# Optimization experiments

Measured on AMD Instinct MI355X. Metric: run time of the kernel, lower is better.

## Reference

```python
import jax, jax.numpy as jnp
import numpy as np

B, S, D, H, DFF = 8, 1024, 1024, 16, 4096
DK = D // H
NEG = -1000000000.0


def layernorm(x, g, b, eps=1e-5):
    mu = jnp.mean(x, axis=-1, keepdims=True)
    var = jnp.mean((x - mu) ** 2, axis=-1, keepdims=True)
    return (x - mu) / jnp.sqrt(var + eps) * g + b


def setup_inputs() -> dict:
    key = jax.random.key(0)
    ks = jax.random.split(key, 16)
    s = 0.02
    inp = {
        "x": jax.random.normal(ks[0], (B, S, D), jnp.float32),
        "binary_mask": jax.random.randint(ks[1], (B, S), 0, 2, jnp.int32),
        # per-head projections stacked: [H, D, DK]
        "Wq": jax.random.normal(ks[2], (H, D, DK), jnp.float32) * s,
        "bq": jnp.zeros((H, DK), jnp.float32),
        "Wk": jax.random.normal(ks[3], (H, D, DK), jnp.float32) * s,
        "bk": jnp.zeros((H, DK), jnp.float32),
        "Wv": jax.random.normal(ks[4], (H, D, DK), jnp.float32) * s,
        "bv": jnp.zeros((H, DK), jnp.float32),
        "Wo": jax.random.normal(ks[5], (D, D), jnp.float32) * s,
        "bo": jnp.zeros((D,), jnp.float32),
        "ga": jnp.ones((D,), jnp.float32),
        "ba": jnp.zeros((D,), jnp.float32),
        "W1": jax.random.normal(ks[6], (D, DFF), jnp.float32) * s,
        "b1": jnp.zeros((DFF,), jnp.float32),
        "W2": jax.random.normal(ks[7], (DFF, D), jnp.float32) * s,
        "b2": jnp.zeros((D,), jnp.float32),
        "gf": jnp.ones((D,), jnp.float32),
        "bf": jnp.zeros((D,), jnp.float32),
    }
    return inp


def encoder_fwd(x, binary_mask, Wq, bq, Wk, bk, Wv, bv, Wo, bo, ga, ba, W1, b1, W2, b2, gf, bf):
    # --- multi-head self-attention (heads vectorized over h axis) ---
    q = jnp.einsum("bsd,hdk->bhsk", x, Wq) + bq[None, :, None, :]
    k = jnp.einsum("bsd,hdk->bhsk", x, Wk) + bk[None, :, None, :]
    v = jnp.einsum("bsd,hdk->bhsk", x, Wv) + bv[None, :, None, :]
    score = jnp.einsum("bhik,bhjk->bhij", q, k) / jnp.sqrt(jnp.float32(DK))
    # mask: binary_mask is over KEY positions, broadcast over query dim
    score = score + jnp.where(binary_mask[:, None, None, :] == 0, NEG, 0.0)
    # NOTE: original code softmaxes over dim=1 of [B,Sq,Sk] -> the QUERY axis
    probs = jax.nn.softmax(score, axis=2)
    ctx = jnp.einsum("bhij,bhjk->bhik", probs, v)  # [B,H,S,DK]
    ctx = jnp.transpose(ctx, (0, 2, 1, 3)).reshape(x.shape[0], x.shape[1], D)
    attn_out = ctx @ Wo + bo
    y = layernorm(x + attn_out, ga, ba)
    # --- FFN ---
    h = jax.nn.relu(y @ W1 + b1)
    ffn_out = h @ W2 + b2
    return layernorm(y + ffn_out, gf, bf)


def reference(x, binary_mask, Wq, bq, Wk, bk, Wv, bv, Wo, bo, ga, ba, W1, b1, W2, b2, gf, bf):
    return encoder_fwd(x, binary_mask, Wq, bq, Wk, bk, Wv, bv, Wo, bo, ga, ba, W1, b1, W2, b2, gf, bf)
```

## Files before the change

### kernel.cpp

```cpp
#include <hip/hip_runtime.h>
#include <hip/hip_bf16.h>

typedef __bf16 bf16;
typedef __bf16 bf16x8 __attribute__((ext_vector_type(8)));
typedef __bf16 bf16x4 __attribute__((ext_vector_type(4)));
typedef float  f32x4  __attribute__((ext_vector_type(4)));

#define NB 8
#define NS 1024
#define ND 1024
#define NH 16
#define NDK 64
#define NDFF 4096

static __device__ __forceinline__ f32x4 mfma16(bf16x8 a, bf16x8 b, f32x4 c) {
    return __builtin_amdgcn_mfma_f32_16x16x32_bf16(a, b, c, 0, 0, 0);
}

#define GLDS(g, l) __builtin_amdgcn_global_load_lds( \
    (const __attribute__((address_space(1))) void*)(g), \
    (__attribute__((address_space(3))) void*)(l), 16, 0, 0)

__global__ __launch_bounds__(256) void cvt_x(const float* __restrict__ in,
                                             bf16* __restrict__ out, int n4)
{
    int idx = blockIdx.x * 256 + threadIdx.x;
    if (idx >= n4) return;
    float4 v = ((const float4*)in)[idx];
    bf16x4 o = { (bf16)v.x, (bf16)v.y, (bf16)v.z, (bf16)v.w };
    ((bf16x4*)out)[idx] = o;
}

__global__ __launch_bounds__(256) void prep_transpose(
    const float* __restrict__ Wq, const float* __restrict__ Wk, const float* __restrict__ Wv,
    const float* __restrict__ Wo, const float* __restrict__ W1, const float* __restrict__ W2,
    bf16* __restrict__ wqkvT, bf16* __restrict__ WoT,
    bf16* __restrict__ W1T, bf16* __restrict__ W2T)
{
    __shared__ float T[64][65];
    int bid = blockIdx.x;
    const float* src; bf16* dst; int srcLd, dstLd, tR, tC; bool scale = false;
    if (bid < 768) {
        int mat = bid >> 4, ty = bid & 15;
        int h = mat & 15, type = mat >> 4;
        const float* W = (type == 0) ? Wq : (type == 1 ? Wk : Wv);
        src = W + (size_t)h * ND * NDK;
        srcLd = NDK; tR = ty * 64; tC = 0;
        dst = wqkvT + ((size_t)type * 1024 + h * 64) * ND;
        dstLd = ND;
        scale = (type == 0);
    } else if (bid < 1024) {
        int b2 = bid - 768; int ty = b2 >> 4, tx = b2 & 15;
        src = Wo; srcLd = ND; tR = ty * 64; tC = tx * 64; dst = WoT; dstLd = ND;
    } else if (bid < 2048) {
        int b2 = bid - 1024; int ty = b2 >> 6, tx = b2 & 63;
        src = W1; srcLd = NDFF; tR = ty * 64; tC = tx * 64; dst = W1T; dstLd = ND;
    } else {
        int b2 = bid - 2048; int ty = b2 >> 4, tx = b2 & 15;
        src = W2; srcLd = ND; tR = ty * 64; tC = tx * 64; dst = W2T; dstLd = NDFF;
    }
    int t = threadIdx.x;
    int c0 = t & 63, r0 = t >> 6;
    #pragma unroll
    for (int rr = 0; rr < 16; rr++) {
        int row = rr * 4 + r0;
        T[row][c0] = src[(size_t)(tR + row) * srcLd + tC + c0];
    }
    __syncthreads();
    #pragma unroll
    for (int cc = 0; cc < 16; cc++) {
        int col = cc * 4 + r0;
        float v = T[c0][col];
        if (scale) v *= 0.125f;
        dst[(size_t)(tC + col) * dstLd + tR + c0] = (bf16)v;
    }
}

__global__ void prep_bias(const float* __restrict__ bq, const float* __restrict__ bk,
                          const float* __restrict__ bv, float* __restrict__ bqkv)
{
    int n = blockIdx.x * 256 + threadIdx.x;
    if (n >= 3072) return;
    int type = n >> 10, hk = n & 1023;
    const float* bb = (type == 0) ? bq : (type == 1 ? bk : bv);
    float v = bb[hk];
    if (type == 0) v *= 0.125f;
    bqkv[n] = v;
}

__device__ __forceinline__ void gemm_bt_core(
    const bf16* __restrict__ A, const bf16* __restrict__ BT, int K,
    int rowBase, int colBase, f32x4 (&acc)[4][4], bf16* As, bf16* Bs)
{
    const int tid = threadIdx.x;
    const int lane = tid & 63, wid = tid >> 6;
    const int wr = (wid >> 1) * 64, wc = (wid & 1) * 64;
    const int lrow = lane & 15, lq = lane >> 4;
    const int srow = wid * 32 + (lane >> 3);
    const int gblk = (lane & 7) ^ ((lane >> 3) & 7);
    const bf16* Arow = A + (size_t)(rowBase + srow) * K + gblk * 8;
    const bf16* Brow = BT + (size_t)(colBase + srow) * K + gblk * 8;
    const int co0 = ((lq) ^ (lrow & 7)) * 8;
    const int co1 = ((4 + lq) ^ (lrow & 7)) * 8;
    f32x4 zz = {0.f, 0.f, 0.f, 0.f};
    #pragma unroll
    for (int i = 0; i < 4; i++)
        #pragma unroll
        for (int j = 0; j < 4; j++) acc[i][j] = zz;
    for (int k0 = 0; k0 < K; k0 += 64) {
        __syncthreads();
        #pragma unroll
        for (int it = 0; it < 4; it++)
            GLDS(Arow + (size_t)it * 8 * K + k0, As + (wid * 32 + it * 8) * 64);
        #pragma unroll
        for (int it = 0; it < 4; it++)
            GLDS(Brow + (size_t)it * 8 * K + k0, Bs + (wid * 32 + it * 8) * 64);
        __syncthreads();
        #pragma unroll
        for (int kh = 0; kh < 2; kh++) {
            const int co = kh ? co1 : co0;
            bf16x8 af[4], bfr[4];
            #pragma unroll
            for (int tt = 0; tt < 4; tt++) {
                af[tt]  = *(const bf16x8*)&As[(wr + tt * 16 + lrow) * 64 + co];
                bfr[tt] = *(const bf16x8*)&Bs[(wc + tt * 16 + lrow) * 64 + co];
            }
            #pragma unroll
            for (int i = 0; i < 4; i++)
                #pragma unroll
                for (int j = 0; j < 4; j++)
                    acc[i][j] = mfma16(af[i], bfr[j], acc[i][j]);
        }
    }
}

__global__ __launch_bounds__(256) void g1_qkv(
    const bf16* __restrict__ x, const bf16* __restrict__ wqkvT, const float* __restrict__ bqkv,
    bf16* __restrict__ Q, bf16* __restrict__ Kb, bf16* __restrict__ Vb)
{
    __shared__ bf16 As[128 * 64], Bs[128 * 64];
    f32x4 acc[4][4];
    int rowBase = blockIdx.x * 128, colBase = blockIdx.y * 128;
    gemm_bt_core(x, wqkvT, ND, rowBase, colBase, acc, As, Bs);
    const int tid = threadIdx.x, lane = tid & 63, wid = tid >> 6;
    const int wr = (wid >> 1) * 64, wc = (wid & 1) * 64, lrow = lane & 15, lq = lane >> 4;
    #pragma unroll
    for (int j = 0; j < 4; j++) {
        int gcol = colBase + wc + j * 16 + lrow;
        float bias = bqkv[gcol];
        int type = gcol >> 10, h = (gcol >> 6) & 15, kk = gcol & 63;
        bf16* dst = (type == 0) ? Q : (type == 1 ? Kb : Vb);
        #pragma unroll
        for (int i = 0; i < 4; i++) {
            #pragma unroll
            for (int r = 0; r < 4; r++) {
                int grow = rowBase + wr + i * 16 + lq * 4 + r;
                int b = grow >> 10, s = grow & 1023;
                dst[((size_t)(b * NH + h) * NS + s) * NDK + kk] = (bf16)(acc[i][j][r] + bias);
            }
        }
    }
}

__global__ __launch_bounds__(256) void vt_trans(
    const bf16* __restrict__ Vb, bf16* __restrict__ Vt)
{
    __shared__ bf16 T[64 * 72];
    int bh = blockIdx.y, s0 = blockIdx.x * 64;
    const bf16* src = Vb + ((size_t)bh * NS + s0) * NDK;
    int tid = threadIdx.x;
    #pragma unroll
    for (int it = 0; it < 2; it++) {
        int g = tid + it * 256;
        int row = g >> 3, c = (g & 7) * 8;
        *(bf16x8*)&T[row * 72 + c] = *(const bf16x8*)&src[row * NDK + c];
    }
    __syncthreads();
    #pragma unroll
    for (int it = 0; it < 2; it++) {
        int g = tid + it * 256;
        int kk = g >> 3, sc = (g & 7) * 8;
        bf16x8 v;
        #pragma unroll
        for (int t = 0; t < 8; t++) v[t] = T[(sc + t) * 72 + kk];
        *(bf16x8*)&Vt[((size_t)bh * NDK + kk) * NS + s0 + sc] = v;
    }
}

__global__ __launch_bounds__(256) void g2_stats(
    const bf16* __restrict__ Q, const bf16* __restrict__ Kb,
    const int* __restrict__ mask, float2* __restrict__ alpha)
{
    __shared__ bf16 Qs[128 * 64];
    int bh = blockIdx.y, b = bh >> 4;
    int jBase = blockIdx.x * 128;
    const bf16* Kp = Kb + (size_t)bh * NS * NDK;
    const bf16* Qp = Q + (size_t)bh * NS * NDK;
    const int tid = threadIdx.x, lane = tid & 63, wid = tid >> 6;
    const int lrow = lane & 15, lq = lane >> 4;
    bf16x8 kf[2][2];
    #pragma unroll
    for (int jt = 0; jt < 2; jt++)
        #pragma unroll
        for (int kh = 0; kh < 2; kh++)
            kf[jt][kh] = *(const bf16x8*)&Kp[(size_t)(jBase + wid * 32 + jt * 16 + lrow) * NDK + kh * 32 + lq * 8];
    const int srow = lane >> 3;
    const int gblk = (lane & 7) ^ srow;
    float Lacc[2][4];
    #pragma unroll
    for (int jt = 0; jt < 2; jt++)
        #pragma unroll
        for (int r = 0; r < 4; r++) Lacc[jt][r] = 0.f;
    f32x4 zz = {0.f, 0.f, 0.f, 0.f};
    for (int i0 = 0; i0 < NS; i0 += 128) {
        __syncthreads();
        #pragma unroll
        for (int it = 0; it < 4; it++)
            GLDS(Qp + (size_t)(i0 + wid * 32 + it * 8 + srow) * NDK + gblk * 8,
                 Qs + (wid * 32 + it * 8) * 64);
        __syncthreads();
        #pragma unroll
        for (int it = 0; it < 8; it++) {
            bf16x8 qb[2];
            #pragma unroll
            for (int kh = 0; kh < 2; kh++)
                qb[kh] = *(const bf16x8*)&Qs[(it * 16 + lrow) * 64 + ((kh * 4 + lq) ^ (lrow & 7)) * 8];
            #pragma unroll
            for (int jt = 0; jt < 2; jt++) {
                f32x4 s = mfma16(kf[jt][0], qb[0], zz);
                s = mfma16(kf[jt][1], qb[1], s);
                #pragma unroll
                for (int r = 0; r < 4; r++) Lacc[jt][r] += __expf(s[r]);
            }
        }
    }
    #pragma unroll
    for (int jt = 0; jt < 2; jt++) {
        #pragma unroll
        for (int r = 0; r < 4; r++) {
            float v = Lacc[jt][r];
            v += __shfl_xor(v, 1); v += __shfl_xor(v, 2);
            v += __shfl_xor(v, 4); v += __shfl_xor(v, 8);
            if (lrow == 0) {
                int j = jBase + wid * 32 + jt * 16 + lq * 4 + r;
                int m = mask[b * NS + j];
                float2 ac;
                ac.x = m ? 1.f / v : 0.f;
                ac.y = m ? 0.f : (1.f / 1024.f);
                alpha[(size_t)bh * NS + j] = ac;
            }
        }
    }
}

__global__ __launch_bounds__(256) void g3_ctx(
    const bf16* __restrict__ Q, const bf16* __restrict__ Kb, const bf16* __restrict__ Vt,
    const float2* __restrict__ alpha, bf16* __restrict__ ctx)
{
    __shared__ bf16 Ks[64 * 64];
    __shared__ bf16 Vs[64 * 64];
    __shared__ bf16 Ps[4 * 64 * 64];
    int bh = blockIdx.y, iBase = blockIdx.x * 256;
    int b = bh >> 4, h = bh & 15;
    const bf16* Qp = Q + (size_t)bh * NS * NDK;
    const bf16* Kp = Kb + (size_t)bh * NS * NDK;
    const bf16* Vp = Vt + (size_t)bh * NDK * NS;
    const float2* al = alpha + (size_t)bh * NS;
    const int tid = threadIdx.x, lane = tid & 63, wid = tid >> 6;
    const int lrow = lane & 15, lq = lane >> 4;
    const int iw = iBase + wid * 64;
    bf16x8 qf[4][2];
    #pragma unroll
    for (int it = 0; it < 4; it++)
        #pragma unroll
        for (int kh = 0; kh < 2; kh++)
            qf[it][kh] = *(const bf16x8*)&Qp[(size_t)(iw + it * 16 + lrow) * NDK + kh * 32 + lq * 8];
    const int srow = lane >> 3;
    const int gblk = (lane & 7) ^ srow;
    f32x4 cacc[4][4];
    f32x4 zz = {0.f, 0.f, 0.f, 0.f};
    #pragma unroll
    for (int it = 0; it < 4; it++)
        #pragma unroll
        for (int kt = 0; kt < 4; kt++) cacc[it][kt] = zz;
    bf16* Pw = Ps + wid * 64 * 64;
    for (int j0 = 0; j0 < NS; j0 += 64) {
        __syncthreads();
        #pragma unroll
        for (int it = 0; it < 2; it++)
            GLDS(Kp + (size_t)(j0 + wid * 16 + it * 8 + srow) * NDK + gblk * 8,
                 Ks + (wid * 16 + it * 8) * 64);
        #pragma unroll
        for (int it = 0; it < 2; it++)
            GLDS(Vp + (size_t)(wid * 16 + it * 8 + srow) * NS + j0 + gblk * 8,
                 Vs + (wid * 16 + it * 8) * 64);
        __syncthreads();
        bf16x8 kb[4][2];
        #pragma unroll
        for (int jt = 0; jt < 4; jt++)
            #pragma unroll
            for (int kh = 0; kh < 2; kh++)
                kb[jt][kh] = *(const bf16x8*)&Ks[(jt * 16 + lrow) * 64 + ((kh * 4 + lq) ^ (lrow & 7)) * 8];
        #pragma unroll
        for (int jt = 0; jt < 4; jt++) {
            float2 acj[4];
            #pragma unroll
            for (int r = 0; r < 4; r++) acj[r] = al[j0 + jt * 16 + lq * 4 + r];
            #pragma unroll
            for (int it = 0; it < 4; it++) {
                f32x4 s = mfma16(kb[jt][0], qf[it][0], zz);
                s = mfma16(kb[jt][1], qf[it][1], s);
                bf16x4 pv;
                #pragma unroll
                for (int r = 0; r < 4; r++)
                    pv[r] = (bf16)(acj[r].x * __expf(s[r]) + acj[r].y);
                int i = it * 16 + lrow;
                int jb = jt * 2 + (lq >> 1);
                *(bf16x4*)&Pw[i * 64 + ((jb ^ (i & 7)) * 8) + (lq & 1) * 4] = pv;
            }
        }
        bf16x8 vb[4][2];
        #pragma unroll
        for (int kt = 0; kt < 4; kt++)
            #pragma unroll
            for (int kh = 0; kh < 2; kh++)
                vb[kt][kh] = *(const bf16x8*)&Vs[(kt * 16 + lrow) * 64 + ((kh * 4 + lq) ^ (lrow & 7)) * 8];
        #pragma unroll
        for (int it = 0; it < 4; it++) {
            bf16x8 pa[2];
            #pragma unroll
            for (int kh = 0; kh < 2; kh++)
                pa[kh] = *(const bf16x8*)&Pw[(it * 16 + lrow) * 64 + ((kh * 4 + lq) ^ (lrow & 7)) * 8];
            #pragma unroll
            for (int kt = 0; kt < 4; kt++) {
                cacc[it][kt] = mfma16(pa[0], vb[kt][0], cacc[it][kt]);
                cacc[it][kt] = mfma16(pa[1], vb[kt][1], cacc[it][kt]);
            }
        }
    }
    #pragma unroll
    for (int kt = 0; kt < 4; kt++) {
        int col = h * NDK + kt * 16 + lrow;
        #pragma unroll
        for (int it = 0; it < 4; it++) {
            #pragma unroll
            for (int r = 0; r < 4; r++) {
                int i = iw + it * 16 + lq * 4 + r;
                ctx[(size_t)(b * NS + i) * ND + col] = (bf16)cacc[it][kt][r];
            }
        }
    }
}

__global__ __launch_bounds__(256) void g4_proj(
    const bf16* __restrict__ ctx, const bf16* __restrict__ WoT, const float* __restrict__ bo,
    const bf16* __restrict__ xb, bf16* __restrict__ t1b)
{
    __shared__ bf16 As[128 * 64], Bs[128 * 64];
    f32x4 acc[4][4];
    int rowBase = blockIdx.x * 128, colBase = blockIdx.y * 128;
    gemm_bt_core(ctx, WoT, ND, rowBase, colBase, acc, As, Bs);
    const int tid = threadIdx.x, lane = tid & 63, wid = tid >> 6;
    const int wr = (wid >> 1) * 64, wc = (wid & 1) * 64, lrow = lane & 15, lq = lane >> 4;
    #pragma unroll
    for (int j = 0; j < 4; j++) {
        int gcol = colBase + wc + j * 16 + lrow;
        float bias = bo[gcol];
        #pragma unroll
        for (int i = 0; i < 4; i++) {
            #pragma unroll
            for (int r = 0; r < 4; r++) {
                int grow = rowBase + wr + i * 16 + lq * 4 + r;
                float v = acc[i][j][r] + bias + (float)xb[(size_t)grow * ND + gcol];
                t1b[(size_t)grow * ND + gcol] = (bf16)v;
            }
        }
    }
}

__global__ __launch_bounds__(256) void g5_ffn1(
    const bf16* __restrict__ y, const bf16* __restrict__ W1T, const float* __restrict__ b1,
    bf16* __restrict__ hb)
{
    __shared__ bf16 As[128 * 64], Bs[128 * 64];
    f32x4 acc[4][4];
    int rowBase = blockIdx.x * 128, colBase = blockIdx.y * 128;
    gemm_bt_core(y, W1T, ND, rowBase, colBase, acc, As, Bs);
    const int tid = threadIdx.x, lane = tid & 63, wid = tid >> 6;
    const int wr = (wid >> 1) * 64, wc = (wid & 1) * 64, lrow = lane & 15, lq = lane >> 4;
    #pragma unroll
    for (int j = 0; j < 4; j++) {
        int gcol = colBase + wc + j * 16 + lrow;
        float bias = b1[gcol];
        #pragma unroll
        for (int i = 0; i < 4; i++) {
            #pragma unroll
            for (int r = 0; r < 4; r++) {
                int grow = rowBase + wr + i * 16 + lq * 4 + r;
                float v = fmaxf(acc[i][j][r] + bias, 0.f);
                hb[(size_t)grow * NDFF + gcol] = (bf16)v;
            }
        }
    }
}

__global__ __launch_bounds__(256) void g6_ffn2(
    const bf16* __restrict__ hb, const bf16* __restrict__ W2T, const float* __restrict__ b2,
    const bf16* __restrict__ yb, bf16* __restrict__ zb)
{
    __shared__ bf16 As[128 * 64], Bs[128 * 64];
    f32x4 acc[4][4];
    int rowBase = blockIdx.x * 128, colBase = blockIdx.y * 128;
    gemm_bt_core(hb, W2T, NDFF, rowBase, colBase, acc, As, Bs);
    const int tid = threadIdx.x, lane = tid & 63, wid = tid >> 6;
    const int wr = (wid >> 1) * 64, wc = (wid & 1) * 64, lrow = lane & 15, lq = lane >> 4;
    #pragma unroll
    for (int j = 0; j < 4; j++) {
        int gcol = colBase + wc + j * 16 + lrow;
        float bias = b2[gcol];
        #pragma unroll
        for (int i = 0; i < 4; i++) {
            #pragma unroll
            for (int r = 0; r < 4; r++) {
                int grow = rowBase + wr + i * 16 + lq * 4 + r;
                float v = acc[i][j][r] + bias + (float)yb[(size_t)grow * ND + gcol];
                zb[(size_t)grow * ND + gcol] = (bf16)v;
            }
        }
    }
}

__global__ __launch_bounds__(256) void ln_kernel(
    const bf16* __restrict__ in, bf16* __restrict__ outb, float* __restrict__ outf,
    const float* __restrict__ g, const float* __restrict__ bb)
{
    int row = blockIdx.x, tid = threadIdx.x;
    const bf16* p = in + (size_t)row * ND;
    bf16x4 v4 = *(const bf16x4*)&p[tid * 4];
    float vv[4] = {(float)v4[0], (float)v4[1], (float)v4[2], (float)v4[3]};
    float s = vv[0] + vv[1] + vv[2] + vv[3];
    float q = vv[0]*vv[0] + vv[1]*vv[1] + vv[2]*vv[2] + vv[3]*vv[3];
    #pragma unroll
    for (int m = 1; m < 64; m <<= 1) { s += __shfl_xor(s, m); q += __shfl_xor(q, m); }
    __shared__ float rs[4], rq[4];
    int wid = tid >> 6, lane = tid & 63;
    if (lane == 0) { rs[wid] = s; rq[wid] = q; }
    __syncthreads();
    s = rs[0] + rs[1] + rs[2] + rs[3];
    q = rq[0] + rq[1] + rq[2] + rq[3];
    float mean = s * (1.f / 1024.f);
    float var = q * (1.f / 1024.f) - mean * mean;
    float rstd = 1.f / sqrtf(var + 1e-5f);
    float4 of;
    bf16x4 ob;
    #pragma unroll
    for (int k = 0; k < 4; k++) {
        int col = tid * 4 + k;
        float yv = (vv[k] - mean) * rstd * g[col] + bb[col];
        ((float*)&of)[k] = yv;
        ob[k] = (bf16)yv;
    }
    if (outb) *(bf16x4*)&outb[(size_t)row * ND + tid * 4] = ob;
    if (outf) ((float4*)(outf + (size_t)row * ND))[tid] = of;
}

extern "C" void kernel_launch(void* const* d_in, const int* in_sizes, int n_in,
                              void* d_out, int out_size, void* d_ws, size_t ws_size,
                              hipStream_t stream)
{
    const float* x    = (const float*)d_in[0];
    const int*   mask = (const int*)d_in[1];
    const float* Wq   = (const float*)d_in[2];
    const float* bq   = (const float*)d_in[3];
    const float* Wk   = (const float*)d_in[4];
    const float* bk   = (const float*)d_in[5];
    const float* Wv   = (const float*)d_in[6];
    const float* bv   = (const float*)d_in[7];
    const float* Wo   = (const float*)d_in[8];
    const float* bo   = (const float*)d_in[9];
    const float* ga   = (const float*)d_in[10];
    const float* ba   = (const float*)d_in[11];
    const float* W1   = (const float*)d_in[12];
    const float* b1   = (const float*)d_in[13];
    const float* W2   = (const float*)d_in[14];
    const float* b2   = (const float*)d_in[15];
    const float* gf   = (const float*)d_in[16];
    const float* bfb  = (const float*)d_in[17];

    size_t off = 0;
    auto alloc = [&](size_t n) { char* p = (char*)d_ws + off; off += (n + 255) & ~(size_t)255; return (void*)p; };
    bf16*   wqkvT = (bf16*)  alloc((size_t)3072 * 1024 * 2);
    bf16*   WoT   = (bf16*)  alloc((size_t)1024 * 1024 * 2);
    bf16*   W1T   = (bf16*)  alloc((size_t)4096 * 1024 * 2);
    bf16*   W2T   = (bf16*)  alloc((size_t)1024 * 4096 * 2);
    float*  bqkv  = (float*) alloc(3072 * 4);
    float2* alpha = (float2*)alloc((size_t)NB * NH * NS * 8);
    bf16*   xb    = (bf16*)  alloc((size_t)8192 * 1024 * 2);
    bf16*   ub    = (bf16*)  alloc((size_t)8192 * 4096 * 2);
    bf16*   Qb    = ub;
    bf16*   Kb    = ub + (size_t)8192 * 1024;
    bf16*   Vt    = ub + (size_t)2 * 8192 * 1024;
    bf16*   ctx   = ub + (size_t)3 * 8192 * 1024;
    bf16*   hb    = ub;
    bf16*   t1b   = (bf16*)  alloc((size_t)8192 * 1024 * 2);
    bf16*   Vb    = t1b;
    bf16*   zb    = t1b;
    bf16*   yb    = (bf16*)  alloc((size_t)8192 * 1024 * 2);

    cvt_x<<<8192, 256, 0, stream>>>(x, xb, 8192 * 1024 / 4);
    prep_transpose<<<3072, 256, 0, stream>>>(Wq, Wk, Wv, Wo, W1, W2, wqkvT, WoT, W1T, W2T);
    prep_bias<<<12, 256, 0, stream>>>(bq, bk, bv, bqkv);
    g1_qkv<<<dim3(64, 24), 256, 0, stream>>>(xb, wqkvT, bqkv, Qb, Kb, Vb);
    vt_trans<<<dim3(16, 128), 256, 0, stream>>>(Vb, Vt);
    g2_stats<<<dim3(8, 128), 256, 0, stream>>>(Qb, Kb, mask, alpha);
    g3_ctx<<<dim3(4, 128), 256, 0, stream>>>(Qb, Kb, Vt, alpha, ctx);
    g4_proj<<<dim3(64, 8), 256, 0, stream>>>(ctx, WoT, bo, xb, t1b);
    ln_kernel<<<8192, 256, 0, stream>>>(t1b, yb, nullptr, ga, ba);
    g5_ffn1<<<dim3(64, 32), 256, 0, stream>>>(yb, W1T, b1, hb);
    g6_ffn2<<<dim3(64, 8), 256, 0, stream>>>(hb, W2T, b2, yb, zb);
    ln_kernel<<<8192, 256, 0, stream>>>(zb, nullptr, (float*)d_out, gf, bfb);
}
```

Baseline: 508.8 us.

## Rewrite GEMM core with 256-row tiles, double-buffered LDS, and XCD-aware block swizzle

Replaces the 128x128 single-buffered GEMM core with a 256xBN (128 or 256) tile run by 512 threads. The next K-tile is prefetched into a second LDS buffer while MFMA clusters interleave with LDS fragment reads under explicit barriers and raised priority. Block indices are remapped with an 8-way swizzle meant to improve L2 locality across XCDs. The aim is to hide global load latency and raise data reuse per tile, at the cost of more LDS and registers, fewer blocks for the smaller GEMMs, and a more fragile barrier schedule.

```diff
diff --git a/kernel.cpp b/kernel.cpp
--- a/kernel.cpp
+++ b/kernel.cpp
@@ -88,73 +88,129 @@
     bqkv[n] = v;
 }
 
-__device__ __forceinline__ void gemm_bt_core(
+template<int BN>
+__device__ __forceinline__ void gemm256_core(
     const bf16* __restrict__ A, const bf16* __restrict__ BT, int K,
-    int rowBase, int colBase, f32x4 (&acc)[4][4], bf16* As, bf16* Bs)
-{
+    int rowBase, int colBase, f32x4 (&acc)[8][BN / 64],
+    bf16* As, bf16* Bs)
+{
+    constexpr int NJ = BN / 128;
+    constexpr int ABUF = 256 * 64;
+    constexpr int BBUF = BN * 64;
     const int tid = threadIdx.x;
     const int lane = tid & 63, wid = tid >> 6;
-    const int wr = (wid >> 1) * 64, wc = (wid & 1) * 64;
+    const int wm = wid >> 2, wn = wid & 3;
     const int lrow = lane & 15, lq = lane >> 4;
-    const int srow = wid * 32 + (lane >> 3);
-    const int gblk = (lane & 7) ^ ((lane >> 3) & 7);
-    const bf16* Arow = A + (size_t)(rowBase + srow) * K + gblk * 8;
-    const bf16* Brow = BT + (size_t)(colBase + srow) * K + gblk * 8;
-    const int co0 = ((lq) ^ (lrow & 7)) * 8;
+    const int srow = lane >> 3, gblk = (lane & 7) ^ srow;
+    const int co0 = (lq ^ (lrow & 7)) * 8;
     const int co1 = ((4 + lq) ^ (lrow & 7)) * 8;
+
     f32x4 zz = {0.f, 0.f, 0.f, 0.f};
     #pragma unroll
-    for (int i = 0; i < 4; i++)
-        #pragma unroll
-        for (int j = 0; j < 4; j++) acc[i][j] = zz;
-    for (int k0 = 0; k0 < K; k0 += 64) {
-        __syncthreads();
-        #pragma unroll
-        for (int it = 0; it < 4; it++)
-            GLDS(Arow + (size_t)it * 8 * K + k0, As + (wid * 32 + it * 8) * 64);
-        #pragma unroll
-        for (int it = 0; it < 4; it++)
-            GLDS(Brow + (size_t)it * 8 * K + k0, Bs + (wid * 32 + it * 8) * 64);
-        __syncthreads();
-        #pragma unroll
-        for (int kh = 0; kh < 2; kh++) {
-            const int co = kh ? co1 : co0;
-            bf16x8 af[4], bfr[4];
-            #pragma unroll
-            for (int tt = 0; tt < 4; tt++) {
-                af[tt]  = *(const bf16x8*)&As[(wr + tt * 16 + lrow) * 64 + co];
-                bfr[tt] = *(const bf16x8*)&Bs[(wc + tt * 16 + lrow) * 64 + co];
-            }
-            #pragma unroll
-            for (int i = 0; i < 4; i++)
-                #pragma unroll
-                for (int j = 0; j < 4; j++)
-                    acc[i][j] = mfma16(af[i], bfr[j], acc[i][j]);
-        }
-    }
-}
-
-__global__ __launch_bounds__(256) void g1_qkv(
+    for (int i = 0; i < 8; i++)
+        #pragma unroll
+        for (int j = 0; j < 2 * NJ; j++) acc[i][j] = zz;
+
+    const bf16* Ag = A  + (size_t)(rowBase + wid * 8 + srow) * K + gblk * 8;
+    const bf16* Bg = BT + (size_t)(colBase + wid * 8 + srow) * K + gblk * 8;
+
+#define STAGE256(kt, bi) do { \
+    const bf16* a_ = Ag + (size_t)(kt) * 64; \
+    _Pragma("unroll") \
+    for (int r_ = 0; r_ < 4; r_++) \
+        GLDS(a_ + (size_t)r_ * 64 * K, As + (bi) * ABUF + (r_ * 64 + wid * 8) * 64); \
+    const bf16* b_ = Bg + (size_t)(kt) * 64; \
+    _Pragma("unroll") \
+    for (int r_ = 0; r_ < BN / 64; r_++) \
+        GLDS(b_ + (size_t)r_ * 64 * K, Bs + (bi) * BBUF + (r_ * 64 + wid * 8) * 64); \
+} while (0)
+
+#define READ_A(MS) \
+    _Pragma("unroll") \
+    for (int i_ = 0; i_ < 4; i_++) { \
+        int ro_ = (wm * 128 + (MS) * 64 + i_ * 16 + lrow) * 64; \
+        af[i_][0] = *(const bf16x8*)&Ab[ro_ + co0]; \
+        af[i_][1] = *(const bf16x8*)&Ab[ro_ + co1]; \
+    }
+
+#define READ_B(NS_) \
+    _Pragma("unroll") \
+    for (int j_ = 0; j_ < NJ; j_++) { \
+        int ro_ = (wn * (BN / 4) + (NS_) * (BN / 8) + j_ * 16 + lrow) * 64; \
+        bfr[j_][0] = *(const bf16x8*)&Bb[ro_ + co0]; \
+        bfr[j_][1] = *(const bf16x8*)&Bb[ro_ + co1]; \
+    }
+
+#define MFMA_CLUSTER(IOFF, JOFF) do { \
+    __builtin_amdgcn_s_barrier(); \
+    asm volatile("s_waitcnt lgkmcnt(0)" ::: "memory"); \
+    __builtin_amdgcn_sched_barrier(0); \
+    __builtin_amdgcn_s_setprio(1); \
+    _Pragma("unroll") \
+    for (int i_ = 0; i_ < 4; i_++) \
+        _Pragma("unroll") \
+        for (int j_ = 0; j_ < NJ; j_++) { \
+            acc[(IOFF) + i_][(JOFF) + j_] = mfma16(af[i_][0], bfr[j_][0], acc[(IOFF) + i_][(JOFF) + j_]); \
+            acc[(IOFF) + i_][(JOFF) + j_] = mfma16(af[i_][1], bfr[j_][1], acc[(IOFF) + i_][(JOFF) + j_]); \
+        } \
+    __builtin_amdgcn_s_setprio(0); \
+} while (0)
+
+    const int nt = K >> 6;
+    STAGE256(0, 0);
+    asm volatile("s_waitcnt vmcnt(0)" ::: "memory");
+    __builtin_amdgcn_s_barrier();
+
+    int cur = 0;
+    for (int t = 0; t < nt; ++t, cur ^= 1) {
+        const bf16* Ab = As + cur * ABUF;
+        const bf16* Bb = Bs + cur * BBUF;
+        bf16x8 af[4][2], bfr[NJ][2];
+        READ_A(0); READ_B(0);
+        if (t + 1 < nt) STAGE256(t + 1, cur ^ 1);
+        MFMA_CLUSTER(0, 0);
+        __builtin_amdgcn_s_barrier();
+        READ_A(1);
+        MFMA_CLUSTER(4, 0);
+        __builtin_amdgcn_s_barrier();
+        READ_B(1);
+        MFMA_CLUSTER(4, NJ);
+        __builtin_amdgcn_s_barrier();
+        READ_A(0);
+        MFMA_CLUSTER(0, NJ);
+        asm volatile("s_waitcnt vmcnt(0)" ::: "memory");
+        __builtin_amdgcn_s_barrier();
+    }
+#undef STAGE256
+#undef READ_A
+#undef READ_B
+#undef MFMA_CLUSTER
+}
+
+__global__ __launch_bounds__(512, 2) void g1_qkv(
     const bf16* __restrict__ x, const bf16* __restrict__ wqkvT, const float* __restrict__ bqkv,
     bf16* __restrict__ Q, bf16* __restrict__ Kb, bf16* __restrict__ Vb)
 {
-    __shared__ bf16 As[128 * 64], Bs[128 * 64];
-    f32x4 acc[4][4];
-    int rowBase = blockIdx.x * 128, colBase = blockIdx.y * 128;
-    gemm_bt_core(x, wqkvT, ND, rowBase, colBase, acc, As, Bs);
+    __shared__ bf16 As[2 * 256 * 64], Bs[2 * 128 * 64];
+    f32x4 acc[8][2];
+    int nwg = gridDim.x, g = blockIdx.x;
+    int sw = (g & 7) * (nwg >> 3) + (g >> 3);
+    int bm = sw / 24, bn = sw % 24;
+    int rowBase = bm * 256, colBase = bn * 128;
+    gemm256_core<128>(x, wqkvT, ND, rowBase, colBase, acc, As, Bs);
     const int tid = threadIdx.x, lane = tid & 63, wid = tid >> 6;
-    const int wr = (wid >> 1) * 64, wc = (wid & 1) * 64, lrow = lane & 15, lq = lane >> 4;
-    #pragma unroll
-    for (int j = 0; j < 4; j++) {
-        int gcol = colBase + wc + j * 16 + lrow;
+    const int wm = wid >> 2, wn = wid & 3, lrow = lane & 15, lq = lane >> 4;
+    #pragma unroll
+    for (int j = 0; j < 2; j++) {
+        int gcol = colBase + wn * 32 + j * 16 + lrow;
         float bias = bqkv[gcol];
         int type = gcol >> 10, h = (gcol >> 6) & 15, kk = gcol & 63;
         bf16* dst = (type == 0) ? Q : (type == 1 ? Kb : Vb);
         #pragma unroll
-        for (int i = 0; i < 4; i++) {
+        for (int i = 0; i < 8; i++) {
             #pragma unroll
             for (int r = 0; r < 4; r++) {
-                int grow = rowBase + wr + i * 16 + lq * 4 + r;
+                int grow = rowBase + wm * 128 + i * 16 + lq * 4 + r;
                 int b = grow >> 10, s = grow & 1023;
                 dst[((size_t)(b * NH + h) * NS + s) * NDK + kk] = (bf16)(acc[i][j][r] + bias);
             }
@@ -352,25 +408,28 @@
     }
 }
 
-__global__ __launch_bounds__(256) void g4_proj(
+__global__ __launch_bounds__(512, 2) void g4_proj(
     const bf16* __restrict__ ctx, const bf16* __restrict__ WoT, const float* __restrict__ bo,
     const bf16* __restrict__ xb, bf16* __restrict__ t1b)
 {
-    __shared__ bf16 As[128 * 64], Bs[128 * 64];
-    f32x4 acc[4][4];
-    int rowBase = blockIdx.x * 128, colBase = blockIdx.y * 128;
-    gemm_bt_core(ctx, WoT, ND, rowBase, colBase, acc, As, Bs);
+    __shared__ bf16 As[2 * 256 * 64], Bs[2 * 128 * 64];
+    f32x4 acc[8][2];
+    int nwg = gridDim.x, g = blockIdx.x;
+    int sw = (g & 7) * (nwg >> 3) + (g >> 3);
+    int bm = sw >> 3, bn = sw & 7;
+    int rowBase = bm * 256, colBase = bn * 128;
+    gemm256_core<128>(ctx, WoT, ND, rowBase, colBase, acc, As, Bs);
     const int tid = threadIdx.x, lane = tid & 63, wid = tid >> 6;
-    const int wr = (wid >> 1) * 64, wc = (wid & 1) * 64, lrow = lane & 15, lq = lane >> 4;
-    #pragma unroll
-    for (int j = 0; j < 4; j++) {
-        int gcol = colBase + wc + j * 16 + lrow;
+    const int wm = wid >> 2, wn = wid & 3, lrow = lane & 15, lq = lane >> 4;
+    #pragma unroll
+    for (int j = 0; j < 2; j++) {
+        int gcol = colBase + wn * 32 + j * 16 + lrow;
         float bias = bo[gcol];
         #pragma unroll
-        for (int i = 0; i < 4; i++) {
+        for (int i = 0; i < 8; i++) {
             #pragma unroll
             for (int r = 0; r < 4; r++) {
-                int grow = rowBase + wr + i * 16 + lq * 4 + r;
+                int grow = rowBase + wm * 128 + i * 16 + lq * 4 + r;
                 float v = acc[i][j][r] + bias + (float)xb[(size_t)grow * ND + gcol];
                 t1b[(size_t)grow * ND + gcol] = (bf16)v;
             }
@@ -378,25 +437,28 @@
     }
 }
 
-__global__ __launch_bounds__(256) void g5_ffn1(
+__global__ __launch_bounds__(512, 2) void g5_ffn1(
     const bf16* __restrict__ y, const bf16* __restrict__ W1T, const float* __restrict__ b1,
     bf16* __restrict__ hb)
 {
-    __shared__ bf16 As[128 * 64], Bs[128 * 64];
-    f32x4 acc[4][4];
-    int rowBase = blockIdx.x * 128, colBase = blockIdx.y * 128;
-    gemm_bt_core(y, W1T, ND, rowBase, colBase, acc, As, Bs);
+    __shared__ bf16 As[2 * 256 * 64], Bs[2 * 256 * 64];
+    f32x4 acc[8][4];
+    int nwg = gridDim.x, g = blockIdx.x;
+    int sw = (g & 7) * (nwg >> 3) + (g >> 3);
+    int bm = sw >> 4, bn = sw & 15;
+    int rowBase = bm * 256, colBase = bn * 256;
+    gemm256_core<256>(y, W1T, ND, rowBase, colBase, acc, As, Bs);
     const int tid = threadIdx.x, lane = tid & 63, wid = tid >> 6;
-    const int wr = (wid >> 1) * 64, wc = (wid & 1) * 64, lrow = lane & 15, lq = lane >> 4;
+    const int wm = wid >> 2, wn = wid & 3, lrow = lane & 15, lq = lane >> 4;
     #pragma unroll
     for (int j = 0; j < 4; j++) {
-        int gcol = colBase + wc + j * 16 + lrow;
+        int gcol = colBase + wn * 64 + j * 16 + lrow;
         float bias = b1[gcol];
         #pragma unroll
-        for (int i = 0; i < 4; i++) {
+        for (int i = 0; i < 8; i++) {
             #pragma unroll
             for (int r = 0; r < 4; r++) {
-                int grow = rowBase + wr + i * 16 + lq * 4 + r;
+                int grow = rowBase + wm * 128 + i * 16 + lq * 4 + r;
                 float v = fmaxf(acc[i][j][r] + bias, 0.f);
                 hb[(size_t)grow * NDFF + gcol] = (bf16)v;
             }
@@ -404,25 +466,28 @@
     }
 }
 
-__global__ __launch_bounds__(256) void g6_ffn2(
+__global__ __launch_bounds__(512, 2) void g6_ffn2(
     const bf16* __restrict__ hb, const bf16* __restrict__ W2T, const float* __restrict__ b2,
     const bf16* __restrict__ yb, bf16* __restrict__ zb)
 {
-    __shared__ bf16 As[128 * 64], Bs[128 * 64];
-    f32x4 acc[4][4];
-    int rowBase = blockIdx.x * 128, colBase = blockIdx.y * 128;
-    gemm_bt_core(hb, W2T, NDFF, rowBase, colBase, acc, As, Bs);
+    __shared__ bf16 As[2 * 256 * 64], Bs[2 * 128 * 64];
+    f32x4 acc[8][2];
+    int nwg = gridDim.x, g = blockIdx.x;
+    int sw = (g & 7) * (nwg >> 3) + (g >> 3);
+    int bm = sw >> 3, bn = sw & 7;
+    int rowBase = bm * 256, colBase = bn * 128;
+    gemm256_core<128>(hb, W2T, NDFF, rowBase, colBase, acc, As, Bs);
     const int tid = threadIdx.x, lane = tid & 63, wid = tid >> 6;
-    const int wr = (wid >> 1) * 64, wc = (wid & 1) * 64, lrow = lane & 15, lq = lane >> 4;
-    #pragma unroll
-    for (int j = 0; j < 4; j++) {
-        int gcol = colBase + wc + j * 16 + lrow;
+    const int wm = wid >> 2, wn = wid & 3, lrow = lane & 15, lq = lane >> 4;
+    #pragma unroll
+    for (int j = 0; j < 2; j++) {
+        int gcol = colBase + wn * 32 + j * 16 + lrow;
         float bias = b2[gcol];
         #pragma unroll
-        for (int i = 0; i < 4; i++) {
+        for (int i = 0; i < 8; i++) {
             #pragma unroll
             for (int r = 0; r < 4; r++) {
-                int grow = rowBase + wr + i * 16 + lq * 4 + r;
+                int grow = rowBase + wm * 128 + i * 16 + lq * 4 + r;
                 float v = acc[i][j][r] + bias + (float)yb[(size_t)grow * ND + gcol];
                 zb[(size_t)grow * ND + gcol] = (bf16)v;
             }
@@ -510,13 +575,13 @@
     cvt_x<<<8192, 256, 0, stream>>>(x, xb, 8192 * 1024 / 4);
     prep_transpose<<<3072, 256, 0, stream>>>(Wq, Wk, Wv, Wo, W1, W2, wqkvT, WoT, W1T, W2T);
     prep_bias<<<12, 256, 0, stream>>>(bq, bk, bv, bqkv);
-    g1_qkv<<<dim3(64, 24), 256, 0, stream>>>(xb, wqkvT, bqkv, Qb, Kb, Vb);
+    g1_qkv<<<768, 512, 0, stream>>>(xb, wqkvT, bqkv, Qb, Kb, Vb);
     vt_trans<<<dim3(16, 128), 256, 0, stream>>>(Vb, Vt);
     g2_stats<<<dim3(8, 128), 256, 0, stream>>>(Qb, Kb, mask, alpha);
     g3_ctx<<<dim3(4, 128), 256, 0, stream>>>(Qb, Kb, Vt, alpha, ctx);
-    g4_proj<<<dim3(64, 8), 256, 0, stream>>>(ctx, WoT, bo, xb, t1b);
+    g4_proj<<<256, 512, 0, stream>>>(ctx, WoT, bo, xb, t1b);
     ln_kernel<<<8192, 256, 0, stream>>>(t1b, yb, nullptr, ga, ba);
-    g5_ffn1<<<dim3(64, 32), 256, 0, stream>>>(yb, W1T, b1, hb);
-    g6_ffn2<<<dim3(64, 8), 256, 0, stream>>>(hb, W2T, b2, yb, zb);
+    g5_ffn1<<<512, 512, 0, stream>>>(yb, W1T, b1, hb);
+    g6_ffn2<<<256, 512, 0, stream>>>(hb, W2T, b2, yb, zb);
     ln_kernel<<<8192, 256, 0, stream>>>(zb, nullptr, (float*)d_out, gf, bfb);
 }
```

After: 566.8 us. 11.4% more time.

## Rewrite FFN GEMMs with larger tiles, 512-thread blocks and multi-stage LDS pipelining

Applied to the files above, without the earlier changes.

Replaces the shared 128x128 GEMM core for the two FFN matmuls with specialized cores. FFN1 uses 256x256 tiles and double buffering, FFN2 uses 128x256 tiles and triple buffering. Both use 8 waves per block, XOR-swizzled LDS, async global-to-LDS loads interleaved with MFMA clusters, setprio, and an XCD-aware block swizzle. The aim is more data reuse per tile and better overlap of memory with compute, at the cost of more registers and LDS per block and finer manual waitcnt handling that could go wrong.

```diff
diff --git a/kernel.cpp b/kernel.cpp
--- a/kernel.cpp
+++ b/kernel.cpp
@@ -378,25 +378,194 @@
     }
 }
 
-__global__ __launch_bounds__(256) void g5_ffn1(
+__device__ __forceinline__ void gemmA_core(
+    const bf16* __restrict__ A, const bf16* __restrict__ BT, int K,
+    int rowBase, int colBase, f32x4 (&acc)[8][4], bf16* As, bf16* Bs)
+{
+    constexpr int ABUF = 256 * 64, BBUF = 256 * 64;
+    const int tid = threadIdx.x, lane = tid & 63, wid = tid >> 6;
+    const int wm = wid >> 2, wn = wid & 3;
+    const int lrow = lane & 15, lq = lane >> 4;
+    const int srow = lane >> 3, gblk = (lane & 7) ^ srow;
+    const int co0 = (lq ^ (lrow & 7)) * 8;
+    const int co1 = ((4 + lq) ^ (lrow & 7)) * 8;
+    f32x4 zz = {0.f, 0.f, 0.f, 0.f};
+    #pragma unroll
+    for (int i = 0; i < 8; i++)
+        #pragma unroll
+        for (int j = 0; j < 4; j++) acc[i][j] = zz;
+    const bf16* Ag = A  + (size_t)(rowBase + wid * 8 + srow) * K + gblk * 8;
+    const bf16* Bg = BT + (size_t)(colBase + wid * 8 + srow) * K + gblk * 8;
+
+#define SGA(kt, bi, rr) GLDS(Ag + (size_t)(kt) * 64 + (size_t)(rr) * 64 * K, \
+                             As + (bi) * ABUF + ((rr) * 64 + wid * 8) * 64)
+#define SGB(kt, bi, rr) GLDS(Bg + (size_t)(kt) * 64 + (size_t)(rr) * 64 * K, \
+                             Bs + (bi) * BBUF + ((rr) * 64 + wid * 8) * 64)
+#define RDA(MS) do { _Pragma("unroll") for (int i_ = 0; i_ < 4; i_++) { \
+    int ro_ = (wm * 128 + (MS) * 64 + i_ * 16 + lrow) * 64; \
+    af[i_][0] = *(const bf16x8*)&Ab[ro_ + co0]; \
+    af[i_][1] = *(const bf16x8*)&Ab[ro_ + co1]; } } while (0)
+#define RDB(dst, NS_) do { _Pragma("unroll") for (int j_ = 0; j_ < 2; j_++) { \
+    int ro_ = (wn * 64 + (NS_) * 32 + j_ * 16 + lrow) * 64; \
+    dst[j_][0] = *(const bf16x8*)&Bb[ro_ + co0]; \
+    dst[j_][1] = *(const bf16x8*)&Bb[ro_ + co1]; } } while (0)
+#define CLUSTER_A(bfx, IO, JO) do { \
+    __builtin_amdgcn_s_barrier(); \
+    asm volatile("s_waitcnt lgkmcnt(0)" ::: "memory"); \
+    __builtin_amdgcn_sched_barrier(0); \
+    __builtin_amdgcn_s_setprio(1); \
+    _Pragma("unroll") \
+    for (int i_ = 0; i_ < 4; i_++) \
+        _Pragma("unroll") \
+        for (int j_ = 0; j_ < 2; j_++) { \
+            acc[(IO) + i_][(JO) + j_] = mfma16(af[i_][0], bfx[j_][0], acc[(IO) + i_][(JO) + j_]); \
+            acc[(IO) + i_][(JO) + j_] = mfma16(af[i_][1], bfx[j_][1], acc[(IO) + i_][(JO) + j_]); \
+        } \
+    __builtin_amdgcn_s_setprio(0); \
+} while (0)
+
+    const int nt = K >> 6;
+    SGA(0, 0, 0); SGA(0, 0, 2);
+    SGB(0, 0, 0); SGB(0, 0, 1); SGB(0, 0, 2); SGB(0, 0, 3);
+    SGA(0, 0, 1); SGA(0, 0, 3);
+    asm volatile("s_waitcnt vmcnt(2)" ::: "memory");
+    __builtin_amdgcn_s_barrier();
+
+    int cur = 0;
+    for (int t = 0; t < nt; ++t, cur ^= 1) {
+        const bf16* Ab = As + cur * ABUF;
+        const bf16* Bb = Bs + cur * BBUF;
+        const bool pf = (t + 1 < nt);
+        bf16x8 af[4][2], bf0[2][2], bf1[2][2];
+        RDA(0); RDB(bf0, 0);
+        if (pf) { SGA(t + 1, cur ^ 1, 0); SGA(t + 1, cur ^ 1, 2); }
+        CLUSTER_A(bf0, 0, 0);
+        __builtin_amdgcn_s_barrier();
+        RDB(bf1, 1);
+        if (pf) { SGB(t + 1, cur ^ 1, 0); SGB(t + 1, cur ^ 1, 1); }
+        CLUSTER_A(bf1, 0, 2);
+        if (pf) asm volatile("s_waitcnt vmcnt(4)" ::: "memory");
+        else    asm volatile("s_waitcnt vmcnt(0)" ::: "memory");
+        __builtin_amdgcn_s_barrier();
+        RDA(1);
+        if (pf) { SGB(t + 1, cur ^ 1, 2); SGB(t + 1, cur ^ 1, 3); }
+        CLUSTER_A(bf1, 4, 2);
+        __builtin_amdgcn_s_barrier();
+        RDB(bf0, 0);
+        if (pf) { SGA(t + 1, cur ^ 1, 1); SGA(t + 1, cur ^ 1, 3); }
+        CLUSTER_A(bf0, 4, 0);
+        if (pf) asm volatile("s_waitcnt vmcnt(2)" ::: "memory");
+        __builtin_amdgcn_s_barrier();
+    }
+#undef SGA
+#undef SGB
+#undef RDA
+#undef RDB
+#undef CLUSTER_A
+}
+
+__device__ __forceinline__ void gemmB_core(
+    const bf16* __restrict__ A, const bf16* __restrict__ BT, int K,
+    int rowBase, int colBase, f32x4 (&acc)[4][4], bf16* As, bf16* Bs)
+{
+    constexpr int ABUF = 128 * 64, BBUF = 256 * 64;
+    const int tid = threadIdx.x, lane = tid & 63, wid = tid >> 6;
+    const int wm = wid >> 2, wn = wid & 3;
+    const int lrow = lane & 15, lq = lane >> 4;
+    const int srow = lane >> 3, gblk = (lane & 7) ^ srow;
+    const int co0 = (lq ^ (lrow & 7)) * 8;
+    const int co1 = ((4 + lq) ^ (lrow & 7)) * 8;
+    f32x4 zz = {0.f, 0.f, 0.f, 0.f};
+    #pragma unroll
+    for (int i = 0; i < 4; i++)
+        #pragma unroll
+        for (int j = 0; j < 4; j++) acc[i][j] = zz;
+    const bf16* Ag = A  + (size_t)(rowBase + wid * 8 + srow) * K + gblk * 8;
+    const bf16* Bg = BT + (size_t)(colBase + wid * 8 + srow) * K + gblk * 8;
+
+#define SGA2(kt, bi, rr) GLDS(Ag + (size_t)(kt) * 64 + (size_t)(rr) * 64 * K, \
+                              As + (bi) * ABUF + ((rr) * 64 + wid * 8) * 64)
+#define SGB2(kt, bi, rr) GLDS(Bg + (size_t)(kt) * 64 + (size_t)(rr) * 64 * K, \
+                              Bs + (bi) * BBUF + ((rr) * 64 + wid * 8) * 64)
+#define RDA2() do { _Pragma("unroll") for (int i_ = 0; i_ < 4; i_++) { \
+    int ro_ = (wm * 64 + i_ * 16 + lrow) * 64; \
+    af[i_][0] = *(const bf16x8*)&Ab[ro_ + co0]; \
+    af[i_][1] = *(const bf16x8*)&Ab[ro_ + co1]; } } while (0)
+#define RDB2(dst, NS_) do { _Pragma("unroll") for (int j_ = 0; j_ < 2; j_++) { \
+    int ro_ = (wn * 64 + (NS_) * 32 + j_ * 16 + lrow) * 64; \
+    dst[j_][0] = *(const bf16x8*)&Bb[ro_ + co0]; \
+    dst[j_][1] = *(const bf16x8*)&Bb[ro_ + co1]; } } while (0)
+#define CLUSTER_B(bfx, JO) do { \
+    __builtin_amdgcn_s_barrier(); \
+    asm volatile("s_waitcnt lgkmcnt(0)" ::: "memory"); \
+    __builtin_amdgcn_sched_barrier(0); \
+    __builtin_amdgcn_s_setprio(1); \
+    _Pragma("unroll") \
+    for (int i_ = 0; i_ < 4; i_++) \
+        _Pragma("unroll") \
+        for (int j_ = 0; j_ < 2; j_++) { \
+            acc[i_][(JO) + j_] = mfma16(af[i_][0], bfx[j_][0], acc[i_][(JO) + j_]); \
+            acc[i_][(JO) + j_] = mfma16(af[i_][1], bfx[j_][1], acc[i_][(JO) + j_]); \
+        } \
+    __builtin_amdgcn_s_setprio(0); \
+} while (0)
+
+    const int nt = K >> 6;
+    SGA2(0, 0, 0); SGA2(0, 0, 1);
+    SGB2(0, 0, 0); SGB2(0, 0, 1); SGB2(0, 0, 2); SGB2(0, 0, 3);
+    SGA2(1, 1, 0); SGA2(1, 1, 1);
+    SGB2(1, 1, 0); SGB2(1, 1, 1); SGB2(1, 1, 2); SGB2(1, 1, 3);
+    asm volatile("s_waitcnt vmcnt(6)" ::: "memory");
+    __builtin_amdgcn_s_barrier();
+
+    int ci = 0, si = 2;
+    for (int t = 0; t < nt; ++t) {
+        const bf16* Ab = As + ci * ABUF;
+        const bf16* Bb = Bs + ci * BBUF;
+        const bool pf = (t + 2 < nt);
+        bf16x8 af[4][2], bf0[2][2], bf1[2][2];
+        RDA2(); RDB2(bf0, 0);
+        if (pf) { SGA2(t + 2, si, 0); SGA2(t + 2, si, 1); SGB2(t + 2, si, 0); SGB2(t + 2, si, 1); }
+        CLUSTER_B(bf0, 0);
+        __builtin_amdgcn_s_barrier();
+        RDB2(bf1, 1);
+        if (pf) { SGB2(t + 2, si, 2); SGB2(t + 2, si, 3); }
+        CLUSTER_B(bf1, 2);
+        if (pf)                asm volatile("s_waitcnt vmcnt(6)" ::: "memory");
+        else if (t + 1 < nt)   asm volatile("s_waitcnt vmcnt(0)" ::: "memory");
+        __builtin_amdgcn_s_barrier();
+        ci = (ci == 2) ? 0 : ci + 1;
+        si = (si == 2) ? 0 : si + 1;
+    }
+#undef SGA2
+#undef SGB2
+#undef RDA2
+#undef RDB2
+#undef CLUSTER_B
+}
+
+__global__ __launch_bounds__(512, 2) void g5_ffn1(
     const bf16* __restrict__ y, const bf16* __restrict__ W1T, const float* __restrict__ b1,
     bf16* __restrict__ hb)
 {
-    __shared__ bf16 As[128 * 64], Bs[128 * 64];
-    f32x4 acc[4][4];
-    int rowBase = blockIdx.x * 128, colBase = blockIdx.y * 128;
-    gemm_bt_core(y, W1T, ND, rowBase, colBase, acc, As, Bs);
-    const int tid = threadIdx.x, lane = tid & 63, wid = tid >> 6;
-    const int wr = (wid >> 1) * 64, wc = (wid & 1) * 64, lrow = lane & 15, lq = lane >> 4;
+    __shared__ bf16 As[2 * 256 * 64], Bs[2 * 256 * 64];
+    f32x4 acc[8][4];
+    int g = blockIdx.x;
+    int sw = (g & 7) * 64 + (g >> 3);
+    int bm = sw >> 4, bn = sw & 15;
+    int rowBase = bm * 256, colBase = bn * 256;
+    gemmA_core(y, W1T, ND, rowBase, colBase, acc, As, Bs);
+    const int tid = threadIdx.x, lane = tid & 63, wid = tid >> 6;
+    const int wm = wid >> 2, wn = wid & 3, lrow = lane & 15, lq = lane >> 4;
     #pragma unroll
     for (int j = 0; j < 4; j++) {
-        int gcol = colBase + wc + j * 16 + lrow;
+        int gcol = colBase + wn * 64 + j * 16 + lrow;
         float bias = b1[gcol];
         #pragma unroll
-        for (int i = 0; i < 4; i++) {
+        for (int i = 0; i < 8; i++) {
             #pragma unroll
             for (int r = 0; r < 4; r++) {
-                int grow = rowBase + wr + i * 16 + lq * 4 + r;
+                int grow = rowBase + wm * 128 + i * 16 + lq * 4 + r;
                 float v = fmaxf(acc[i][j][r] + bias, 0.f);
                 hb[(size_t)grow * NDFF + gcol] = (bf16)v;
             }
@@ -404,25 +573,28 @@
     }
 }
 
-__global__ __launch_bounds__(256) void g6_ffn2(
+__global__ __launch_bounds__(512, 2) void g6_ffn2(
     const bf16* __restrict__ hb, const bf16* __restrict__ W2T, const float* __restrict__ b2,
     const bf16* __restrict__ yb, bf16* __restrict__ zb)
 {
-    __shared__ bf16 As[128 * 64], Bs[128 * 64];
+    __shared__ bf16 As[3 * 128 * 64], Bs[3 * 256 * 64];
     f32x4 acc[4][4];
-    int rowBase = blockIdx.x * 128, colBase = blockIdx.y * 128;
-    gemm_bt_core(hb, W2T, NDFF, rowBase, colBase, acc, As, Bs);
-    const int tid = threadIdx.x, lane = tid & 63, wid = tid >> 6;
-    const int wr = (wid >> 1) * 64, wc = (wid & 1) * 64, lrow = lane & 15, lq = lane >> 4;
+    int g = blockIdx.x;
+    int sw = (g & 7) * 32 + (g >> 3);
+    int bm = sw >> 2, bn = sw & 3;
+    int rowBase = bm * 128, colBase = bn * 256;
+    gemmB_core(hb, W2T, NDFF, rowBase, colBase, acc, As, Bs);
+    const int tid = threadIdx.x, lane = tid & 63, wid = tid >> 6;
+    const int wm = wid >> 2, wn = wid & 3, lrow = lane & 15, lq = lane >> 4;
     #pragma unroll
     for (int j = 0; j < 4; j++) {
-        int gcol = colBase + wc + j * 16 + lrow;
+        int gcol = colBase + wn * 64 + j * 16 + lrow;
         float bias = b2[gcol];
         #pragma unroll
         for (int i = 0; i < 4; i++) {
             #pragma unroll
             for (int r = 0; r < 4; r++) {
-                int grow = rowBase + wr + i * 16 + lq * 4 + r;
+                int grow = rowBase + wm * 64 + i * 16 + lq * 4 + r;
                 float v = acc[i][j][r] + bias + (float)yb[(size_t)grow * ND + gcol];
                 zb[(size_t)grow * ND + gcol] = (bf16)v;
             }
@@ -516,7 +688,7 @@
     g3_ctx<<<dim3(4, 128), 256, 0, stream>>>(Qb, Kb, Vt, alpha, ctx);
     g4_proj<<<dim3(64, 8), 256, 0, stream>>>(ctx, WoT, bo, xb, t1b);
     ln_kernel<<<8192, 256, 0, stream>>>(t1b, yb, nullptr, ga, ba);
-    g5_ffn1<<<dim3(64, 32), 256, 0, stream>>>(yb, W1T, b1, hb);
-    g6_ffn2<<<dim3(64, 8), 256, 0, stream>>>(hb, W2T, b2, yb, zb);
+    g5_ffn1<<<512, 512, 0, stream>>>(yb, W1T, b1, hb);
+    g6_ffn2<<<256, 512, 0, stream>>>(hb, W2T, b2, yb, zb);
     ln_kernel<<<8192, 256, 0, stream>>>(zb, nullptr, (float*)d_out, gf, bfb);
 }
```

Result: no change. 501.7 us (-1.4%).
